# Kernel optimization log

Hardware: AMD Instinct MI355X
Metric: run time of the kernel (lower is better)

The kernel has to match this reference:

```python
import jax, jax.numpy as jnp
import numpy as np

ROPE_BASE = 10000.0
CHUNK = 2048
NEG_INF = -1e30


def _rope(q, k, start_index):
    # q, k: (B, T, H, Dh) with Dh even; half-split RoPE as in RotaryEmbedding
    B, T, H, Dh = q.shape
    half = Dh // 2
    inv_freq = jnp.exp(jnp.arange(half, dtype=jnp.float32) * (-(np.log(ROPE_BASE) / half)))
    pos = jnp.arange(T, dtype=jnp.float32) + jnp.float32(start_index)
    ang = pos[:, None] * inv_freq[None, :]              # (T, half)
    cos = jnp.cos(ang)[None, :, None, :].astype(q.dtype)  # (1,T,1,half)
    sin = jnp.sin(ang)[None, :, None, :].astype(q.dtype)

    def rot(x):
        x1, x2 = x[..., :half], x[..., half:]
        return jnp.concatenate([x1 * cos - x2 * sin, x2 * cos + x1 * sin], axis=-1)

    return rot(q), rot(k)


def reference(q, k, v, start_index):
    # Chunked causal self-attention, softmax(QK^T) V with scale = 1.0 (Megalodon Eq. 9).
    B, T, H, Dh = q.shape
    Dv = v.shape[-1]
    q, k = _rope(q, k, start_index)

    nc = T // CHUNK  # T assumed multiple of chunk_size (prefill path, no cache)
    qc = q.reshape(B, nc, CHUNK, H, Dh)
    kc = k.reshape(B, nc, CHUNK, H, Dh)
    vc = v.reshape(B, nc, CHUNK, H, Dv)

    # per-chunk causal mask (C, C): 0 where j <= i else -inf
    i = jnp.arange(CHUNK)
    causal = (i[None, :] <= i[:, None])

    scores = jnp.einsum('bnqhd,bnkhd->bnhqk', qc, kc)  # scale = 1.0
    scores = jnp.where(causal[None, None, None, :, :], scores, NEG_INF)
    probs = jax.nn.softmax(scores, axis=-1)
    out = jnp.einsum('bnhqk,bnkhd->bnqhd', probs, vc)
    return out.reshape(B, T, H, Dv)


def setup_inputs() -> dict:
    key = jax.random.key(0)
    kq, kk, kv = jax.random.split(key, 3)
    B, T, H, Dh, Dv = 2, 4096, 16, 128, 128
    return {
        'q': jax.random.normal(kq, (B, T, H, Dh), dtype=jnp.float32),
        'k': jax.random.normal(kk, (B, T, H, Dh), dtype=jnp.float32),
        'v': jax.random.normal(kv, (B, T, H, Dv), dtype=jnp.float32),
        'start_index': 0,
    }
```

## Files before the change

kernel.cpp:

```cpp
#include <hip/hip_runtime.h>


#define T_TOT  4096
#define HH     16
#define DH     128
#define CHUNKL 2048
#define KTILE  64
#define NEGV   1e30f
#define L2E    1.44269504088896f
#define THRL2  11.5415603f

typedef _Float16 f16;
typedef __attribute__((ext_vector_type(8)))  _Float16 f16x8;
typedef __attribute__((ext_vector_type(4)))  _Float16 f16x4;
typedef __attribute__((ext_vector_type(4)))  float    f32x4;

#define AS_G(p) ((const __attribute__((address_space(1))) void*)(p))
#define AS_L(p) ((__attribute__((address_space(3))) void*)(p))

__device__ __forceinline__ f32x4 mfma16(f16x8 a, f16x8 b, f32x4 c) {
    return __builtin_amdgcn_mfma_f32_16x16x32_f16(a, b, c, 0, 0, 0);
}

__global__ void rope_table_kernel(float* __restrict__ tab, const int* __restrict__ startp) {
    int gid = blockIdx.x * blockDim.x + threadIdx.x;
    int t = gid >> 6, d = gid & 63;
    float pos  = (float)(t + *startp);
    float invf = expf((float)d * (-9.210340371976184f / 64.0f));
    float s, c;
    sincosf(pos * invf, &s, &c);
    tab[gid] = c;
    tab[T_TOT * 64 + gid] = s;
}

__global__ void prep_kv_kernel(const float* __restrict__ K, const float* __restrict__ V,
                               const float* __restrict__ tab,
                               f16* __restrict__ Kws, f16* __restrict__ VTws) {
    const int half = (2 * T_TOT * HH * DH) / 8;
    int gid = blockIdx.x * blockDim.x + threadIdx.x;
    if (gid < half) {
        const int tile = gid >> 10, idx = gid & 1023;
        const int key = idx >> 4, c8 = idx & 15;
        const int dsw0 = c8 << 3;
        const int d0   = dsw0 ^ ((key & 15) << 3);
        const int kt = tile & 31, h = (tile >> 5) & 15, n = (tile >> 9) & 1, b = tile >> 10;
        const int t  = n * CHUNKL + kt * KTILE + key;
        const float* kp = K + ((size_t)(b * T_TOT + t) * HH + h) * DH;
        const int dl = d0 & 63;
        f32x4 xm0 = *(const f32x4*)(kp + d0);
        f32x4 xm1 = *(const f32x4*)(kp + d0 + 4);
        f32x4 xo0 = *(const f32x4*)(kp + (d0 ^ 64));
        f32x4 xo1 = *(const f32x4*)(kp + (d0 ^ 64) + 4);
        f32x4 cc0 = *(const f32x4*)(tab + t * 64 + dl);
        f32x4 cc1 = *(const f32x4*)(tab + t * 64 + dl + 4);
        f32x4 ss0 = *(const f32x4*)(tab + T_TOT * 64 + t * 64 + dl);
        f32x4 ss1 = *(const f32x4*)(tab + T_TOT * 64 + t * 64 + dl + 4);
        const float sgn = (d0 < 64) ? -1.f : 1.f;
        f16x8 out;
#pragma unroll
        for (int j = 0; j < 4; ++j) {
            out[j]     = (f16)(xm0[j] * cc0[j] + sgn * xo0[j] * ss0[j]);
            out[4 + j] = (f16)(xm1[j] * cc1[j] + sgn * xo1[j] * ss1[j]);
        }
        *(f16x8*)&Kws[(size_t)tile * 8192 + key * DH + dsw0] = out;
    } else {
        const int oc = gid - half;
        const int tile = oc >> 10, idx = oc & 1023;
        const int d = idx >> 3, c8 = idx & 7;
        const int ksw0 = c8 << 3;
        const int key0 = ksw0 ^ ((d & 7) << 3);
        const int kt = tile & 31, h = (tile >> 5) & 15, n = (tile >> 9) & 1, b = tile >> 10;
        const int t0 = n * CHUNKL + kt * KTILE + key0;
        const float* vp = V + ((size_t)(b * T_TOT + t0) * HH + h) * DH + d;
        f16x8 out;
#pragma unroll
        for (int j = 0; j < 8; ++j)
            out[j] = (f16)vp[(size_t)j * (HH * DH)];
        *(f16x8*)&VTws[(size_t)tile * 8192 + d * KTILE + ksw0] = out;
    }
}

__global__ __launch_bounds__(256, 4)
void attn_fast_kernel(const float* __restrict__ Q, const f16* __restrict__ Kws,
                      const f16* __restrict__ VTws, const float* __restrict__ tab,
                      float* __restrict__ O)
{
    __shared__ f16 Kl[KTILE * DH];
    __shared__ f16 VTl[KTILE * DH];
    __shared__ f16 Pl[4][16 * 64];

    const int bid = blockIdx.x;
    const int xcd = bid & 7;
    const int idx = bid >> 3;
    const int r   = idx >> 5;
    const int c   = idx & 31;
    const int base = (c + 8 * (r >> 1)) & 31;
    const int qt  = (r & 1) ? (31 - base) : base;
    const int bnh = xcd * 8 + r;
    const int hd = bnh & 15, n = (bnh >> 4) & 1, b = bnh >> 5;

    const int tid = threadIdx.x;
    const int w   = tid >> 6;
    const int l   = tid & 63;
    const int g   = l >> 4;
    const int m   = l & 15;

    const int q0 = qt * 64;
    const size_t bh = (size_t)b * T_TOT * (HH * DH) + (size_t)hd * DH;
    const size_t tile0 = (size_t)bnh * (32 * 8192);

    const int qr = q0 + w * 16 + m;
    const int tg = n * CHUNKL + qr;
    const float* qp = Q + bh + (size_t)tg * (HH * DH);

    f16x8 qf[4];
#pragma unroll
    for (int kc = 0; kc < 4; ++kc) {
        const int dbase = kc * 32 + g * 8;
        const int dl    = dbase & 63;
        f32x4 xa0 = *(const f32x4*)(qp + dbase);
        f32x4 xa1 = *(const f32x4*)(qp + dbase + 4);
        f32x4 xb0 = *(const f32x4*)(qp + (dbase ^ 64));
        f32x4 xb1 = *(const f32x4*)(qp + (dbase ^ 64) + 4);
        float cc[8], ss[8];
        *(f32x4*)&cc[0] = *(const f32x4*)(tab + tg * 64 + dl);
        *(f32x4*)&cc[4] = *(const f32x4*)(tab + tg * 64 + dl + 4);
        *(f32x4*)&ss[0] = *(const f32x4*)(tab + T_TOT * 64 + tg * 64 + dl);
        *(f32x4*)&ss[4] = *(const f32x4*)(tab + T_TOT * 64 + tg * 64 + dl + 4);
        const float sgn = (dbase < 64) ? -1.f : 1.f;
        float xa[8] = {xa0[0],xa0[1],xa0[2],xa0[3],xa1[0],xa1[1],xa1[2],xa1[3]};
        float xb[8] = {xb0[0],xb0[1],xb0[2],xb0[3],xb1[0],xb1[1],xb1[2],xb1[3]};
        f16x8 f;
#pragma unroll
        for (int j = 0; j < 8; ++j)
            f[j] = (f16)((xa[j] * cc[j] + sgn * xb[j] * ss[j]) * L2E);
        qf[kc] = f;
    }

    f32x4 o[8];
    float mrun = -NEGV, lrun = 0.f;
    const f32x4 ZERO4 = {0.f, 0.f, 0.f, 0.f};
#pragma unroll
    for (int dt = 0; dt < 8; ++dt) o[dt] = ZERO4;

    const int nkt = qt + 1;

    for (int kt = 0; kt < nkt; ++kt) {
        {
            const f16* ks_ = Kws  + tile0 + (size_t)kt * 8192;
            const f16* vs_ = VTws + tile0 + (size_t)kt * 8192;
#pragma unroll
            for (int i = 0; i < 4; ++i) {
                __builtin_amdgcn_global_load_lds(AS_G(ks_ + i * 2048 + tid * 8),
                                                 AS_L(&Kl[i * 2048 + tid * 8]), 16, 0, 0);
                __builtin_amdgcn_global_load_lds(AS_G(vs_ + i * 2048 + tid * 8),
                                                 AS_L(&VTl[i * 2048 + tid * 8]), 16, 0, 0);
            }
        }
        __syncthreads();

        const bool active = (kt * KTILE) < (q0 + w * 16 + 16);
        if (active) {
            f32x4 s[4];
#pragma unroll
            for (int ts = 0; ts < 4; ++ts) s[ts] = ZERO4;

            __builtin_amdgcn_s_setprio(1);
#pragma unroll
            for (int kc = 0; kc < 4; ++kc) {
#pragma unroll
                for (int ts = 0; ts < 4; ++ts) {
                    const int key = ts * 16 + m;
                    f16x8 kf = *(const f16x8*)&Kl[key * DH + ((kc * 32 + 8 * g) ^ (m * 8))];
                    s[ts] = mfma16(kf, qf[kc], s[ts]);
                }
            }
            __builtin_amdgcn_s_setprio(0);

            if ((kt + 1) * KTILE > q0 + w * 16) {
#pragma unroll
                for (int ts = 0; ts < 4; ++ts)
#pragma unroll
                    for (int rr = 0; rr < 4; ++rr) {
                        const int key = kt * KTILE + ts * 16 + 4 * g + rr;
                        if (key > qr) s[ts][rr] = -NEGV;
                    }
            }

            float ma = fmaxf(fmaxf(s[0][0], s[0][1]), fmaxf(s[0][2], s[0][3]));
            float mb = fmaxf(fmaxf(s[1][0], s[1][1]), fmaxf(s[1][2], s[1][3]));
            float mc = fmaxf(fmaxf(s[2][0], s[2][1]), fmaxf(s[2][2], s[2][3]));
            float md = fmaxf(fmaxf(s[3][0], s[3][1]), fmaxf(s[3][2], s[3][3]));
            float mx = fmaxf(fmaxf(ma, mb), fmaxf(mc, md));
            mx = fmaxf(mx, __shfl_xor(mx, 16));
            mx = fmaxf(mx, __shfl_xor(mx, 32));

            if (__any(mx > mrun + THRL2)) {
                const float mn = fmaxf(mrun, mx);
                const float al = exp2f(mrun - mn);
                mrun = mn;
                lrun *= al;
#pragma unroll
                for (int dt = 0; dt < 8; ++dt)
#pragma unroll
                    for (int rr = 0; rr < 4; ++rr) o[dt][rr] *= al;
            }

#pragma unroll
            for (int ts = 0; ts < 4; ++ts)
#pragma unroll
                for (int rr = 0; rr < 4; ++rr) s[ts][rr] = exp2f(s[ts][rr] - mrun);
            {
                float p0 = (s[0][0] + s[0][1]) + (s[0][2] + s[0][3]);
                float p1 = (s[1][0] + s[1][1]) + (s[1][2] + s[1][3]);
                float p2 = (s[2][0] + s[2][1]) + (s[2][2] + s[2][3]);
                float p3 = (s[3][0] + s[3][1]) + (s[3][2] + s[3][3]);
                lrun += (p0 + p1) + (p2 + p3);
            }

#pragma unroll
            for (int ts = 0; ts < 4; ++ts) {
                f16x4 pk;
                pk[0] = (f16)s[ts][0];
                pk[1] = (f16)s[ts][1];
                pk[2] = (f16)s[ts][2];
                pk[3] = (f16)s[ts][3];
                const int blk = (2 * ts + (g >> 1)) ^ (m & 7);
                *(f16x4*)&Pl[w][m * 64 + blk * 8 + (g & 1) * 4] = pk;
            }

            __builtin_amdgcn_s_setprio(1);
#pragma unroll
            for (int kc = 0; kc < 2; ++kc) {
                f16x8 pb = *(const f16x8*)&Pl[w][m * 64 + ((kc * 4 + g) ^ (m & 7)) * 8];
#pragma unroll
                for (int dt = 0; dt < 8; ++dt) {
                    const int d = dt * 16 + m;
                    f16x8 vf = *(const f16x8*)&VTl[d * KTILE + ((kc * 32 + 8 * g) ^ ((m & 7) * 8))];
                    o[dt] = mfma16(vf, pb, o[dt]);
                }
            }
            __builtin_amdgcn_s_setprio(0);
        }

        __syncthreads();
    }

    float lt = lrun;
    lt += __shfl_xor(lt, 16);
    lt += __shfl_xor(lt, 32);
    const float inv = 1.0f / lt;
    float* op = O + bh + (size_t)tg * (HH * DH);
#pragma unroll
    for (int dt = 0; dt < 8; ++dt) {
        f32x4 val;
#pragma unroll
        for (int rr = 0; rr < 4; ++rr) val[rr] = o[dt][rr] * inv;
        *(f32x4*)&op[dt * 16 + 4 * g] = val;
    }
}

__global__ __launch_bounds__(256, 2)
void attn_kernel(const float* __restrict__ Q, const float* __restrict__ K,
                 const float* __restrict__ V, const int* __restrict__ startp,
                 float* __restrict__ O)
{
    __shared__ f16 Kl[KTILE * DH];
    __shared__ f16 VTl[DH * KTILE];
    __shared__ f16 Pl[4][32 * 72];

    const int bid = blockIdx.x;
    const int qt  = 15 - (bid & 15);
    const int bnh = bid >> 4;
    const int h = bnh & 15, n = (bnh >> 4) & 1, b = bnh >> 5;

    const int tid  = threadIdx.x;
    const int w    = tid >> 6;
    const int lane = tid & 63;
    const int g    = lane >> 4, m = lane & 15;

    const int q0 = qt * 128;
    const size_t bh = (size_t)b * T_TOT * (HH * DH) + (size_t)h * DH;
    const int start = *startp;

    f16x8  qf[2][4];
    float  mrun[2][4], lrun[2][4];
    f32x4  o[2][8];
    const f32x4 ZERO4 = {0.f, 0.f, 0.f, 0.f};

#pragma unroll
    for (int rs = 0; rs < 2; ++rs) {
#pragma unroll
        for (int r = 0; r < 4; ++r) { mrun[rs][r] = -NEGV; lrun[rs][r] = 0.f; }
#pragma unroll
        for (int dt = 0; dt < 8; ++dt) o[rs][dt] = ZERO4;

        const int tg = n * CHUNKL + q0 + w * 32 + rs * 16 + m;
        const float* qp = Q + bh + (size_t)tg * (HH * DH);
#pragma unroll
        for (int kc = 0; kc < 4; ++kc) {
            const int dbase = kc * 32 + g * 8;
            const int dlo   = dbase & 63;
            f32x4 xa0 = *(const f32x4*)(qp + dbase);
            f32x4 xa1 = *(const f32x4*)(qp + dbase + 4);
            f32x4 xb0 = *(const f32x4*)(qp + (dbase ^ 64));
            f32x4 xb1 = *(const f32x4*)(qp + (dbase ^ 64) + 4);
            float cc[8], ss[8];
#pragma unroll
            for (int j = 0; j < 8; ++j) {
                float invf = expf((float)(dlo + j) * (-9.210340371976184f / 64.0f));
                sincosf((float)(tg + start) * invf, &ss[j], &cc[j]);
            }
            const float sgn = (dbase < 64) ? -1.f : 1.f;
            float xa[8] = {xa0[0],xa0[1],xa0[2],xa0[3],xa1[0],xa1[1],xa1[2],xa1[3]};
            float xb[8] = {xb0[0],xb0[1],xb0[2],xb0[3],xb1[0],xb1[1],xb1[2],xb1[3]};
            f16x8 f;
#pragma unroll
            for (int j = 0; j < 8; ++j) f[j] = (f16)(xa[j] * cc[j] + sgn * xb[j] * ss[j]);
            qf[rs][kc] = f;
        }
    }

    const int nkt = 2 * qt + 2;
    for (int kt = 0; kt < nkt; ++kt) {
        __syncthreads();
#pragma unroll
        for (int it = 0; it < 4; ++it) {
            const int tau = tid + 256 * it;
            const int row = tau >> 4;
            const int d0  = (tau & 15) << 2;
            const int tg  = n * CHUNKL + kt * KTILE + row;
            const float* kp = K + bh + (size_t)tg * (HH * DH);
            f32x4 xa = *(const f32x4*)(kp + d0);
            f32x4 xb = *(const f32x4*)(kp + d0 + 64);
            f32x4 cc, ss;
#pragma unroll
            for (int j = 0; j < 4; ++j) {
                float invf = expf((float)(d0 + j) * (-9.210340371976184f / 64.0f));
                float sv, cv;
                sincosf((float)(tg + start) * invf, &sv, &cv);
                cc[j] = cv; ss[j] = sv;
            }
            f16x4 oA, oB;
#pragma unroll
            for (int j = 0; j < 4; ++j) {
                oA[j] = (f16)(xa[j] * cc[j] - xb[j] * ss[j]);
                oB[j] = (f16)(xb[j] * cc[j] + xa[j] * ss[j]);
            }
            const int sw = (row & 7) << 3;
            *(f16x4*)&Kl[row * DH + (d0 ^ sw)]        = oA;
            *(f16x4*)&Kl[row * DH + ((d0 + 64) ^ sw)] = oB;
        }
#pragma unroll
        for (int it = 0; it < 8; ++it) {
            const int tau = tid + 256 * it;
            const int key = tau & 63;
            const int d0  = (tau >> 6) << 2;
            const int tg  = n * CHUNKL + kt * KTILE + key;
            f32x4 x = *(const f32x4*)(V + bh + (size_t)tg * (HH * DH) + d0);
#pragma unroll
            for (int j = 0; j < 4; ++j) {
                const int d = d0 + j;
                VTl[d * KTILE + (key ^ ((d & 7) << 3))] = (f16)x[j];
            }
        }
        __syncthreads();

        const bool active = (kt * KTILE) < (q0 + w * 32 + 32);
        if (active) {
            f32x4 sa[2][4];
#pragma unroll
            for (int rs = 0; rs < 2; ++rs)
#pragma unroll
                for (int nt = 0; nt < 4; ++nt) sa[rs][nt] = ZERO4;
#pragma unroll
            for (int nt = 0; nt < 4; ++nt) {
                const int key = nt * 16 + m;
                const int swk = (key & 7) << 3;
#pragma unroll
                for (int kc = 0; kc < 4; ++kc) {
                    f16x8 bf = *(const f16x8*)&Kl[key * DH + ((kc * 32 + g * 8) ^ swk)];
                    sa[0][nt] = mfma16(qf[0][kc], bf, sa[0][nt]);
                    sa[1][nt] = mfma16(qf[1][kc], bf, sa[1][nt]);
                }
            }
            const bool domask = (kt >= 2 * qt);
#pragma unroll
            for (int rs = 0; rs < 2; ++rs) {
                if (domask) {
#pragma unroll
                    for (int nt = 0; nt < 4; ++nt) {
                        const int key = kt * KTILE + nt * 16 + m;
#pragma unroll
                        for (int r = 0; r < 4; ++r) {
                            const int qr = q0 + w * 32 + rs * 16 + 4 * g + r;
                            if (key > qr) sa[rs][nt][r] = -NEGV;
                        }
                    }
                }
                float mx[4];
#pragma unroll
                for (int r = 0; r < 4; ++r)
                    mx[r] = fmaxf(fmaxf(sa[rs][0][r], sa[rs][1][r]),
                                  fmaxf(sa[rs][2][r], sa[rs][3][r]));
#pragma unroll
                for (int off = 1; off < 16; off <<= 1)
#pragma unroll
                    for (int r = 0; r < 4; ++r)
                        mx[r] = fmaxf(mx[r], __shfl_xor(mx[r], off));
                float al[4], ps[4];
#pragma unroll
                for (int r = 0; r < 4; ++r) {
                    const float mn = fmaxf(mrun[rs][r], mx[r]);
                    al[r] = exp2f((mrun[rs][r] - mn) * L2E);
                    mrun[rs][r] = mn;
                    ps[r] = 0.f;
                }
#pragma unroll
                for (int nt = 0; nt < 4; ++nt)
#pragma unroll
                    for (int r = 0; r < 4; ++r) {
                        const float p = exp2f((sa[rs][nt][r] - mrun[rs][r]) * L2E);
                        sa[rs][nt][r] = p;
                        ps[r] += p;
                    }
#pragma unroll
                for (int off = 1; off < 16; off <<= 1)
#pragma unroll
                    for (int r = 0; r < 4; ++r)
                        ps[r] += __shfl_xor(ps[r], off);
#pragma unroll
                for (int r = 0; r < 4; ++r)
                    lrun[rs][r] = lrun[rs][r] * al[r] + ps[r];
#pragma unroll
                for (int dt = 0; dt < 8; ++dt)
#pragma unroll
                    for (int r = 0; r < 4; ++r)
                        o[rs][dt][r] *= al[r];
#pragma unroll
                for (int nt = 0; nt < 4; ++nt)
#pragma unroll
                    for (int r = 0; r < 4; ++r)
                        Pl[w][(rs * 16 + 4 * g + r) * 72 + nt * 16 + m] = (f16)sa[rs][nt][r];
            }
            f16x8 pa[2][2];
#pragma unroll
            for (int rs = 0; rs < 2; ++rs)
#pragma unroll
                for (int kc = 0; kc < 2; ++kc)
                    pa[rs][kc] = *(const f16x8*)&Pl[w][(rs * 16 + m) * 72 + kc * 32 + g * 8];
#pragma unroll
            for (int dt = 0; dt < 8; ++dt) {
                const int d   = dt * 16 + m;
                const int swv = (d & 7) << 3;
#pragma unroll
                for (int kc = 0; kc < 2; ++kc) {
                    f16x8 vf = *(const f16x8*)&VTl[d * KTILE + ((kc * 32 + g * 8) ^ swv)];
                    o[0][dt] = mfma16(pa[0][kc], vf, o[0][dt]);
                    o[1][dt] = mfma16(pa[1][kc], vf, o[1][dt]);
                }
            }
        }
    }

#pragma unroll
    for (int rs = 0; rs < 2; ++rs) {
#pragma unroll
        for (int r = 0; r < 4; ++r) {
            const float inv = 1.0f / lrun[rs][r];
            const int tg = n * CHUNKL + q0 + w * 32 + rs * 16 + 4 * g + r;
            float* op = O + bh + (size_t)tg * (HH * DH);
#pragma unroll
            for (int dt = 0; dt < 8; ++dt)
                op[dt * 16 + m] = o[rs][dt][r] * inv;
        }
    }
}

extern "C" void kernel_launch(void* const* d_in, const int* in_sizes, int n_in,
                              void* d_out, int out_size, void* d_ws, size_t ws_size,
                              hipStream_t stream) {
    const float* q = (const float*)d_in[0];
    const float* k = (const float*)d_in[1];
    const float* v = (const float*)d_in[2];
    const int* start = (const int*)d_in[3];
    float* out = (float*)d_out;

    const size_t tab_elems = (size_t)2 * T_TOT * 64;
    const size_t kv_elems  = (size_t)2 * T_TOT * HH * DH;
    const size_t need = tab_elems * sizeof(float) + 2 * kv_elems * sizeof(f16);

    if (ws_size >= need) {
        float* tab = (float*)d_ws;
        f16* Kws  = (f16*)((char*)d_ws + tab_elems * sizeof(float));
        f16* VTws = Kws + kv_elems;
        rope_table_kernel<<<(T_TOT * 64) / 256, 256, 0, stream>>>(tab, start);
        prep_kv_kernel<<<(int)(2 * (kv_elems / 8) / 256), 256, 0, stream>>>(k, v, tab, Kws, VTws);
        attn_fast_kernel<<<2048, 256, 0, stream>>>(q, Kws, VTws, tab, out);
    } else {
        attn_kernel<<<64 * 16, 256, 0, stream>>>(q, k, v, start, out);
    }
}
```

Before: 204.6 us.

## Halve attention key tile to 32 and raise occupancy with simpler block mapping

Shrinks the fast-path key tile from 64 to 32 keys. This halves LDS per block and lets launch bounds request 8 blocks per SM, with matching changes to the prepacked K/V^T layouts and swizzles. The block-to-tile mapping is simplified to a reversed-qt order grouped by head within each XCD, replacing the previous balanced interleave. The aim is more overlap and finer causal work granularity. In exchange it pays twice as many loop iterations and syncs, and register pressure at 8 waves-per-SIMD bounds could cause spills.

Result: slower. 454.6 us (median of 2 runs) (+122.2%).

```diff
diff --git a/kernel.cpp b/kernel.cpp
--- a/kernel.cpp
+++ b/kernel.cpp
@@ -5,7 +5,8 @@
 #define HH     16
 #define DH     128
 #define CHUNKL 2048
-#define KTILE  64
+#define KTILE  32
+#define FKT    64
 #define NEGV   1e30f
 #define L2E    1.44269504088896f
 #define THRL2  11.5415603f
@@ -39,11 +40,11 @@
     const int half = (2 * T_TOT * HH * DH) / 8;
     int gid = blockIdx.x * blockDim.x + threadIdx.x;
     if (gid < half) {
-        const int tile = gid >> 10, idx = gid & 1023;
+        const int tile = gid >> 9, idx = gid & 511;
         const int key = idx >> 4, c8 = idx & 15;
         const int dsw0 = c8 << 3;
         const int d0   = dsw0 ^ ((key & 15) << 3);
-        const int kt = tile & 31, h = (tile >> 5) & 15, n = (tile >> 9) & 1, b = tile >> 10;
+        const int kt = tile & 63, h = (tile >> 6) & 15, n = (tile >> 10) & 1, b = tile >> 11;
         const int t  = n * CHUNKL + kt * KTILE + key;
         const float* kp = K + ((size_t)(b * T_TOT + t) * HH + h) * DH;
         const int dl = d0 & 63;
@@ -62,41 +63,37 @@
             out[j]     = (f16)(xm0[j] * cc0[j] + sgn * xo0[j] * ss0[j]);
             out[4 + j] = (f16)(xm1[j] * cc1[j] + sgn * xo1[j] * ss1[j]);
         }
-        *(f16x8*)&Kws[(size_t)tile * 8192 + key * DH + dsw0] = out;
+        *(f16x8*)&Kws[(size_t)tile * 4096 + key * DH + dsw0] = out;
     } else {
         const int oc = gid - half;
-        const int tile = oc >> 10, idx = oc & 1023;
-        const int d = idx >> 3, c8 = idx & 7;
+        const int tile = oc >> 9, idx = oc & 511;
+        const int d = idx >> 2, c8 = idx & 3;
         const int ksw0 = c8 << 3;
-        const int key0 = ksw0 ^ ((d & 7) << 3);
-        const int kt = tile & 31, h = (tile >> 5) & 15, n = (tile >> 9) & 1, b = tile >> 10;
+        const int key0 = ksw0 ^ ((d & 3) << 3);
+        const int kt = tile & 63, h = (tile >> 6) & 15, n = (tile >> 10) & 1, b = tile >> 11;
         const int t0 = n * CHUNKL + kt * KTILE + key0;
         const float* vp = V + ((size_t)(b * T_TOT + t0) * HH + h) * DH + d;
         f16x8 out;
 #pragma unroll
         for (int j = 0; j < 8; ++j)
             out[j] = (f16)vp[(size_t)j * (HH * DH)];
-        *(f16x8*)&VTws[(size_t)tile * 8192 + d * KTILE + ksw0] = out;
-    }
-}
-
-__global__ __launch_bounds__(256, 4)
+        *(f16x8*)&VTws[(size_t)tile * 4096 + d * KTILE + ksw0] = out;
+    }
+}
+
+__global__ __launch_bounds__(256, 8)
 void attn_fast_kernel(const float* __restrict__ Q, const f16* __restrict__ Kws,
                       const f16* __restrict__ VTws, const float* __restrict__ tab,
                       float* __restrict__ O)
 {
     __shared__ f16 Kl[KTILE * DH];
-    __shared__ f16 VTl[KTILE * DH];
-    __shared__ f16 Pl[4][16 * 64];
+    __shared__ f16 VTl[DH * KTILE];
+    __shared__ f16 Pl[4][16 * 32];
 
     const int bid = blockIdx.x;
-    const int xcd = bid & 7;
-    const int idx = bid >> 3;
-    const int r   = idx >> 5;
-    const int c   = idx & 31;
-    const int base = (c + 8 * (r >> 1)) & 31;
-    const int qt  = (r & 1) ? (31 - base) : base;
-    const int bnh = xcd * 8 + r;
+    const int sb  = (bid & 7) * 256 + (bid >> 3);
+    const int qt  = 31 - (sb & 31);
+    const int bnh = sb >> 5;
     const int hd = bnh & 15, n = (bnh >> 4) & 1, b = bnh >> 5;
 
     const int tid = threadIdx.x;
@@ -107,7 +104,7 @@
 
     const int q0 = qt * 64;
     const size_t bh = (size_t)b * T_TOT * (HH * DH) + (size_t)hd * DH;
-    const size_t tile0 = (size_t)bnh * (32 * 8192);
+    const size_t tile0 = (size_t)bnh * (64 * 4096);
 
     const int qr = q0 + w * 16 + m;
     const int tg = n * CHUNKL + qr;
@@ -143,14 +140,14 @@
 #pragma unroll
     for (int dt = 0; dt < 8; ++dt) o[dt] = ZERO4;
 
-    const int nkt = qt + 1;
+    const int nkt = 2 * qt + 2;
 
     for (int kt = 0; kt < nkt; ++kt) {
         {
-            const f16* ks_ = Kws  + tile0 + (size_t)kt * 8192;
-            const f16* vs_ = VTws + tile0 + (size_t)kt * 8192;
-#pragma unroll
-            for (int i = 0; i < 4; ++i) {
+            const f16* ks_ = Kws  + tile0 + (size_t)kt * 4096;
+            const f16* vs_ = VTws + tile0 + (size_t)kt * 4096;
+#pragma unroll
+            for (int i = 0; i < 2; ++i) {
                 __builtin_amdgcn_global_load_lds(AS_G(ks_ + i * 2048 + tid * 8),
                                                  AS_L(&Kl[i * 2048 + tid * 8]), 16, 0, 0);
                 __builtin_amdgcn_global_load_lds(AS_G(vs_ + i * 2048 + tid * 8),
@@ -161,15 +158,14 @@
 
         const bool active = (kt * KTILE) < (q0 + w * 16 + 16);
         if (active) {
-            f32x4 s[4];
-#pragma unroll
-            for (int ts = 0; ts < 4; ++ts) s[ts] = ZERO4;
+            f32x4 s[2];
+            s[0] = ZERO4; s[1] = ZERO4;
 
             __builtin_amdgcn_s_setprio(1);
 #pragma unroll
             for (int kc = 0; kc < 4; ++kc) {
 #pragma unroll
-                for (int ts = 0; ts < 4; ++ts) {
+                for (int ts = 0; ts < 2; ++ts) {
                     const int key = ts * 16 + m;
                     f16x8 kf = *(const f16x8*)&Kl[key * DH + ((kc * 32 + 8 * g) ^ (m * 8))];
                     s[ts] = mfma16(kf, qf[kc], s[ts]);
@@ -179,7 +175,7 @@
 
             if ((kt + 1) * KTILE > q0 + w * 16) {
 #pragma unroll
-                for (int ts = 0; ts < 4; ++ts)
+                for (int ts = 0; ts < 2; ++ts)
 #pragma unroll
                     for (int rr = 0; rr < 4; ++rr) {
                         const int key = kt * KTILE + ts * 16 + 4 * g + rr;
@@ -189,9 +185,7 @@
 
             float ma = fmaxf(fmaxf(s[0][0], s[0][1]), fmaxf(s[0][2], s[0][3]));
             float mb = fmaxf(fmaxf(s[1][0], s[1][1]), fmaxf(s[1][2], s[1][3]));
-            float mc = fmaxf(fmaxf(s[2][0], s[2][1]), fmaxf(s[2][2], s[2][3]));
-            float md = fmaxf(fmaxf(s[3][0], s[3][1]), fmaxf(s[3][2], s[3][3]));
-            float mx = fmaxf(fmaxf(ma, mb), fmaxf(mc, md));
+            float mx = fmaxf(ma, mb);
             mx = fmaxf(mx, __shfl_xor(mx, 16));
             mx = fmaxf(mx, __shfl_xor(mx, 32));
 
@@ -207,38 +201,33 @@
             }
 
 #pragma unroll
-            for (int ts = 0; ts < 4; ++ts)
+            for (int ts = 0; ts < 2; ++ts)
 #pragma unroll
                 for (int rr = 0; rr < 4; ++rr) s[ts][rr] = exp2f(s[ts][rr] - mrun);
             {
                 float p0 = (s[0][0] + s[0][1]) + (s[0][2] + s[0][3]);
                 float p1 = (s[1][0] + s[1][1]) + (s[1][2] + s[1][3]);
-                float p2 = (s[2][0] + s[2][1]) + (s[2][2] + s[2][3]);
-                float p3 = (s[3][0] + s[3][1]) + (s[3][2] + s[3][3]);
-                lrun += (p0 + p1) + (p2 + p3);
-            }
-
-#pragma unroll
-            for (int ts = 0; ts < 4; ++ts) {
+                lrun += p0 + p1;
+            }
+
+#pragma unroll
+            for (int ts = 0; ts < 2; ++ts) {
                 f16x4 pk;
                 pk[0] = (f16)s[ts][0];
                 pk[1] = (f16)s[ts][1];
                 pk[2] = (f16)s[ts][2];
                 pk[3] = (f16)s[ts][3];
-                const int blk = (2 * ts + (g >> 1)) ^ (m & 7);
-                *(f16x4*)&Pl[w][m * 64 + blk * 8 + (g & 1) * 4] = pk;
-            }
-
+                const int blk = (ts * 4 + g) ^ (m & 6);
+                *(f16x4*)&Pl[w][m * 32 + blk * 4] = pk;
+            }
+
+            f16x8 pb = *(const f16x8*)&Pl[w][m * 32 + ((2 * g) ^ (m & 6)) * 4];
             __builtin_amdgcn_s_setprio(1);
 #pragma unroll
-            for (int kc = 0; kc < 2; ++kc) {
-                f16x8 pb = *(const f16x8*)&Pl[w][m * 64 + ((kc * 4 + g) ^ (m & 7)) * 8];
-#pragma unroll
-                for (int dt = 0; dt < 8; ++dt) {
-                    const int d = dt * 16 + m;
-                    f16x8 vf = *(const f16x8*)&VTl[d * KTILE + ((kc * 32 + 8 * g) ^ ((m & 7) * 8))];
-                    o[dt] = mfma16(vf, pb, o[dt]);
-                }
+            for (int dt = 0; dt < 8; ++dt) {
+                const int d = dt * 16 + m;
+                f16x8 vf = *(const f16x8*)&VTl[d * KTILE + ((8 * g) ^ ((d & 3) * 8))];
+                o[dt] = mfma16(vf, pb, o[dt]);
             }
             __builtin_amdgcn_s_setprio(0);
         }
@@ -265,8 +254,8 @@
                  const float* __restrict__ V, const int* __restrict__ startp,
                  float* __restrict__ O)
 {
-    __shared__ f16 Kl[KTILE * DH];
-    __shared__ f16 VTl[DH * KTILE];
+    __shared__ f16 Kl[FKT * DH];
+    __shared__ f16 VTl[DH * FKT];
     __shared__ f16 Pl[4][32 * 72];
 
     const int bid = blockIdx.x;
@@ -329,7 +318,7 @@
             const int tau = tid + 256 * it;
             const int row = tau >> 4;
             const int d0  = (tau & 15) << 2;
-            const int tg  = n * CHUNKL + kt * KTILE + row;
+            const int tg  = n * CHUNKL + kt * FKT + row;
             const float* kp = K + bh + (size_t)tg * (HH * DH);
             f32x4 xa = *(const f32x4*)(kp + d0);
             f32x4 xb = *(const f32x4*)(kp + d0 + 64);
@@ -356,17 +345,17 @@
             const int tau = tid + 256 * it;
             const int key = tau & 63;
             const int d0  = (tau >> 6) << 2;
-            const int tg  = n * CHUNKL + kt * KTILE + key;
+            const int tg  = n * CHUNKL + kt * FKT + key;
             f32x4 x = *(const f32x4*)(V + bh + (size_t)tg * (HH * DH) + d0);
 #pragma unroll
             for (int j = 0; j < 4; ++j) {
                 const int d = d0 + j;
-                VTl[d * KTILE + (key ^ ((d & 7) << 3))] = (f16)x[j];
+                VTl[d * FKT + (key ^ ((d & 7) << 3))] = (f16)x[j];
             }
         }
         __syncthreads();
 
-        const bool active = (kt * KTILE) < (q0 + w * 32 + 32);
+        const bool active = (kt * FKT) < (q0 + w * 32 + 32);
         if (active) {
             f32x4 sa[2][4];
 #pragma unroll
@@ -390,7 +379,7 @@
                 if (domask) {
 #pragma unroll
                     for (int nt = 0; nt < 4; ++nt) {
-                        const int key = kt * KTILE + nt * 16 + m;
+                        const int key = kt * FKT + nt * 16 + m;
 #pragma unroll
                         for (int r = 0; r < 4; ++r) {
                             const int qr = q0 + w * 32 + rs * 16 + 4 * g + r;
@@ -455,7 +444,7 @@
                 const int swv = (d & 7) << 3;
 #pragma unroll
                 for (int kc = 0; kc < 2; ++kc) {
-                    f16x8 vf = *(const f16x8*)&VTl[d * KTILE + ((kc * 32 + g * 8) ^ swv)];
+                    f16x8 vf = *(const f16x8*)&VTl[d * FKT + ((kc * 32 + g * 8) ^ swv)];
                     o[0][dt] = mfma16(pa[0][kc], vf, o[0][dt]);
                     o[1][dt] = mfma16(pa[1][kc], vf, o[1][dt]);
                 }
```
